# Kernel optimization log

Hardware: AMD Instinct MI355X
Metric: run time of the kernel (lower is better)

## Reference

```python
import jax, jax.numpy as jnp
import numpy as np

B, V = 256, 2048
PD, MD, H = 1024, 512, 512

def setup_inputs() -> dict:
    key = jax.random.key(0)
    k1, k2, k3, k4, k5 = jax.random.split(key, 5)
    patient_emb = jax.random.normal(k1, (B, PD), dtype=jnp.float32)
    atc4_emb = jax.random.normal(k2, (V, MD), dtype=jnp.float32)
    # Linear(PD+MD -> H): weight (H, PD+MD), bias (H,)
    W1 = jax.random.normal(k3, (H, PD + MD), dtype=jnp.float32) * 0.02
    b1 = jnp.zeros((H,), dtype=jnp.float32)
    # Linear(H -> 1): weight (1, H) -> store as (H,), bias scalar
    w2 = jax.random.normal(k4, (H,), dtype=jnp.float32) * 0.05
    b2 = jnp.zeros((), dtype=jnp.float32)
    return {"patient_emb": patient_emb, "atc4_emb": atc4_emb,
            "W1": W1, "b1": b1, "w2": w2, "b2": b2}

def reference(patient_emb, atc4_emb, W1, b1, w2, b2):
    # Algebraically equivalent to cat([patient, mol]) @ W1.T:
    # split W1 into patient and mol blocks, matmul each, broadcast-add.
    W1p = W1[:, :PD]   # (H, PD)
    W1m = W1[:, PD:]   # (H, MD)
    hp = jnp.einsum('bp,hp->bh', patient_emb, W1p)   # (B, H)
    hm = jnp.einsum('vm,hm->vh', atc4_emb, W1m)      # (V, H)
    h = jnp.tanh(hp[:, None, :] + hm[None, :, :] + b1)  # (B, V, H)
    scores = jnp.einsum('bvh,h->bv', h, w2) + b2     # (B, V)
    return scores
```

## Files before the change

### kernel.cpp

```cpp
#include <hip/hip_runtime.h>
#include <hip/hip_bf16.h>
#include <math.h>

typedef __attribute__((ext_vector_type(8))) short short8;
typedef __attribute__((ext_vector_type(4))) float float4v;
typedef __attribute__((ext_vector_type(2))) float float2v;

__device__ __forceinline__ float2v lo2(float4v v) {
    return __builtin_shufflevector(v, v, 0, 1);
}
__device__ __forceinline__ float2v hi2(float4v v) {
    return __builtin_shufflevector(v, v, 2, 3);
}

__device__ __forceinline__ int2 cvt2bf16x4(float4v v) {
    union { __hip_bfloat162 h2; int i; } u0, u1;
    u0.h2 = __float22bfloat162_rn(make_float2(v.x, v.y));
    u1.h2 = __float22bfloat162_rn(make_float2(v.z, v.w));
    return make_int2(u0.i, u1.i);
}

__global__ __launch_bounds__(256, 2) void gemm_exp(
    const float* __restrict__ patient, const float* __restrict__ atc4,
    const float* __restrict__ W1, const float* __restrict__ b1,
    float* __restrict__ EA, float* __restrict__ EM)
{
    const float* A; const float* W; const float* bias; float* T;
    int lda, K, M;
    int bx = blockIdx.x;
    if (bx < 4) {
        A = patient; lda = 1024; K = 1024; M = 256; bias = b1; T = EA; W = W1;
    } else {
        bx -= 4;
        A = atc4;    lda = 512;  K = 512;  M = 2048; bias = nullptr; T = EM; W = W1 + 1024;
    }
    const int ldw = 1536;

    __shared__ short As[64][72];
    __shared__ short Bs[64][72];
    const int t = threadIdx.x;
    const int m0 = bx * 64;
    const int n0 = blockIdx.y * 64;
    const int wave = t >> 6;
    const int lane = t & 63;
    const int wm = (wave & 1) * 32;
    const int wn = (wave >> 1) * 32;
    const int lrow = lane & 15;
    const int quad = lane >> 4;

    float4v acc[2][2];
    #pragma unroll
    for (int i = 0; i < 2; i++)
        #pragma unroll
        for (int j = 0; j < 2; j++)
            acc[i][j] = (float4v){0.f, 0.f, 0.f, 0.f};

    const int sr = t >> 2;
    const int sc = (t & 3) * 16;

    float4v av[4], wv[4];
    {
        const float* ap = A + (size_t)(m0 + sr) * lda + sc;
        const float* wp = W + (size_t)(n0 + sr) * ldw + sc;
        #pragma unroll
        for (int ii = 0; ii < 4; ii++) {
            av[ii] = *(const float4v*)(ap + ii * 4);
            wv[ii] = *(const float4v*)(wp + ii * 4);
        }
    }

    for (int k0 = 0; k0 < K; k0 += 64) {
        #pragma unroll
        for (int ii = 0; ii < 4; ii++) {
            *(int2*)&As[sr][sc + ii * 4] = cvt2bf16x4(av[ii]);
            *(int2*)&Bs[sr][sc + ii * 4] = cvt2bf16x4(wv[ii]);
        }
        __syncthreads();
        if (k0 + 64 < K) {
            const float* ap = A + (size_t)(m0 + sr) * lda + (k0 + 64 + sc);
            const float* wp = W + (size_t)(n0 + sr) * ldw + (k0 + 64 + sc);
            #pragma unroll
            for (int ii = 0; ii < 4; ii++) {
                av[ii] = *(const float4v*)(ap + ii * 4);
                wv[ii] = *(const float4v*)(wp + ii * 4);
            }
        }
        #pragma unroll
        for (int kk = 0; kk < 64; kk += 32) {
            short8 af[2], bfr[2];
            #pragma unroll
            for (int i = 0; i < 2; i++)
                af[i] = *(const short8*)&As[wm + i * 16 + lrow][kk + quad * 8];
            #pragma unroll
            for (int j = 0; j < 2; j++)
                bfr[j] = *(const short8*)&Bs[wn + j * 16 + lrow][kk + quad * 8];
            #pragma unroll
            for (int i = 0; i < 2; i++)
                #pragma unroll
                for (int j = 0; j < 2; j++)
                    acc[i][j] = __builtin_amdgcn_mfma_f32_16x16x32_bf16(
                        af[i], bfr[j], acc[i][j], 0, 0, 0);
        }
        __syncthreads();
    }

    #pragma unroll
    for (int i = 0; i < 2; i++) {
        #pragma unroll
        for (int j = 0; j < 2; j++) {
            const int n  = n0 + wn + j * 16 + lrow;
            const int mb = m0 + wm + i * 16 + quad * 4;
            const float bn = bias ? bias[n] : 0.0f;
            float4v ev;
            #pragma unroll
            for (int r = 0; r < 4; r++)
                ev[r] = __expf(2.0f * (acc[i][j][r] + bn));
            *(float4v*)&T[(size_t)n * M + mb] = ev;
        }
    }
}

__device__ __forceinline__ void rat4(
    float2v em0, float2v em1, float2v em2, float2v em3,
    float2v a0, float2v a1, float2v a2, float2v a3,
    float2v c0, float2v c1, float2v c2, float2v c3,
    float2v& acc)
{
    const float2v one2 = {1.f, 1.f};
    float2v d0 = __builtin_elementwise_fma(em0, a0, one2);
    float2v d1 = __builtin_elementwise_fma(em1, a1, one2);
    float2v d2 = __builtin_elementwise_fma(em2, a2, one2);
    float2v d3 = __builtin_elementwise_fma(em3, a3, one2);
    float2v e01 = d0 * d1;
    float2v e23 = d2 * d3;
    float2v n01 = __builtin_elementwise_fma(d1, c0, d0 * c1);
    float2v n23 = __builtin_elementwise_fma(d3, c2, d2 * c3);
    float2v num = __builtin_elementwise_fma(n01, e23, n23 * e01);
    float2v den = e01 * e23;
    float2v r = { __builtin_amdgcn_rcpf(den.x), __builtin_amdgcn_rcpf(den.y) };
    acc = __builtin_elementwise_fma(num, r, acc);
}

__global__ __launch_bounds__(256, 4) void pair_kernel(
    const float* __restrict__ EA, const float* __restrict__ EM,
    const float* __restrict__ w2, float* __restrict__ partial)
{
    __shared__ float sEA[32][68];
    __shared__ float sEM[32][132];
    __shared__ float4v sC4[8];
    const int t  = threadIdx.x;
    const int v0 = blockIdx.x * 128;
    const int b0 = blockIdx.y * 64;
    const int h0 = blockIdx.z * 32;
    const int tx = t & 15;
    const int ty = t >> 4;

    if (t < 8) {
        float4v wvq = *(const float4v*)(w2 + h0 + 4 * t);
        sC4[t] = -2.0f * wvq;
    }

    float2v accAL[4], accAH[4], accBL[4], accBH[4];
    #pragma unroll
    for (int i = 0; i < 4; i++) {
        accAL[i] = (float2v){0.f, 0.f};  accAH[i] = (float2v){0.f, 0.f};
        accBL[i] = (float2v){0.f, 0.f};  accBH[i] = (float2v){0.f, 0.f};
    }

    const int rS = t >> 3;
    const int cA = (t & 7) * 8;
    const int cM = (t & 7) * 16;

    {
        const float* pa = EA + (size_t)(h0 + rS) * 256 + b0 + cA;
        float4v pA0 = *(const float4v*)pa;
        float4v pA1 = *(const float4v*)(pa + 4);
        const float* pm = EM + (size_t)(h0 + rS) * 2048 + v0 + cM;
        float4v pM0 = *(const float4v*)pm;
        float4v pM1 = *(const float4v*)(pm + 4);
        float4v pM2 = *(const float4v*)(pm + 8);
        float4v pM3 = *(const float4v*)(pm + 12);
        *(float4v*)&sEA[rS][cA] = pA0;      *(float4v*)&sEA[rS][cA + 4] = pA1;
        *(float4v*)&sEM[rS][cM] = pM0;      *(float4v*)&sEM[rS][cM + 4] = pM1;
        *(float4v*)&sEM[rS][cM + 8] = pM2;  *(float4v*)&sEM[rS][cM + 12] = pM3;
    }
    __syncthreads();

    #pragma unroll 2
    for (int q = 0; q < 8; q++) {
        const int hq = 4 * q;
        const float4v ea0 = *(const float4v*)&sEA[hq    ][ty * 4];
        const float4v ea1 = *(const float4v*)&sEA[hq + 1][ty * 4];
        const float4v ea2 = *(const float4v*)&sEA[hq + 2][ty * 4];
        const float4v ea3 = *(const float4v*)&sEA[hq + 3][ty * 4];
        const float4v c = sC4[q];
        const float2v c0 = { c.x, c.x };
        const float2v c1 = { c.y, c.y };
        const float2v c2 = { c.z, c.z };
        const float2v c3 = { c.w, c.w };
        {
            const float4v em0 = *(const float4v*)&sEM[hq    ][tx * 4];
            const float4v em1 = *(const float4v*)&sEM[hq + 1][tx * 4];
            const float4v em2 = *(const float4v*)&sEM[hq + 2][tx * 4];
            const float4v em3 = *(const float4v*)&sEM[hq + 3][tx * 4];
            const float2v em0L = lo2(em0), em0H = hi2(em0);
            const float2v em1L = lo2(em1), em1H = hi2(em1);
            const float2v em2L = lo2(em2), em2H = hi2(em2);
            const float2v em3L = lo2(em3), em3H = hi2(em3);
            #pragma unroll
            for (int i = 0; i < 4; i++) {
                const float2v a0 = { ea0[i], ea0[i] };
                const float2v a1 = { ea1[i], ea1[i] };
                const float2v a2 = { ea2[i], ea2[i] };
                const float2v a3 = { ea3[i], ea3[i] };
                rat4(em0L, em1L, em2L, em3L, a0, a1, a2, a3,
                     c0, c1, c2, c3, accAL[i]);
                rat4(em0H, em1H, em2H, em3H, a0, a1, a2, a3,
                     c0, c1, c2, c3, accAH[i]);
            }
        }
        {
            const float4v em0 = *(const float4v*)&sEM[hq    ][64 + tx * 4];
            const float4v em1 = *(const float4v*)&sEM[hq + 1][64 + tx * 4];
            const float4v em2 = *(const float4v*)&sEM[hq + 2][64 + tx * 4];
            const float4v em3 = *(const float4v*)&sEM[hq + 3][64 + tx * 4];
            const float2v em0L = lo2(em0), em0H = hi2(em0);
            const float2v em1L = lo2(em1), em1H = hi2(em1);
            const float2v em2L = lo2(em2), em2H = hi2(em2);
            const float2v em3L = lo2(em3), em3H = hi2(em3);
            #pragma unroll
            for (int i = 0; i < 4; i++) {
                const float2v a0 = { ea0[i], ea0[i] };
                const float2v a1 = { ea1[i], ea1[i] };
                const float2v a2 = { ea2[i], ea2[i] };
                const float2v a3 = { ea3[i], ea3[i] };
                rat4(em0L, em1L, em2L, em3L, a0, a1, a2, a3,
                     c0, c1, c2, c3, accBL[i]);
                rat4(em0H, em1H, em2H, em3H, a0, a1, a2, a3,
                     c0, c1, c2, c3, accBH[i]);
            }
        }
    }

    float4v w2q = sC4[0];
    #pragma unroll
    for (int k = 1; k < 8; k++) w2q += sC4[k];
    const float w2s = -0.5f * (w2q.x + w2q.y + w2q.z + w2q.w);

    const size_t pb = (size_t)blockIdx.z * (256 * 2048);
    #pragma unroll
    for (int i = 0; i < 4; i++) {
        const size_t row = pb + (size_t)(b0 + ty * 4 + i) * 2048 + v0 + tx * 4;
        float4v oA = { accAL[i].x + w2s, accAL[i].y + w2s,
                       accAH[i].x + w2s, accAH[i].y + w2s };
        float4v oB = { accBL[i].x + w2s, accBL[i].y + w2s,
                       accBH[i].x + w2s, accBH[i].y + w2s };
        *(float4v*)&partial[row] = oA;
        *(float4v*)&partial[row + 64] = oB;
    }
}

__global__ __launch_bounds__(256) void reduce_kernel(
    const float* __restrict__ partial, const float* __restrict__ b2,
    float* __restrict__ out)
{
    const int i = (blockIdx.x * 256 + threadIdx.x) * 4;
    const float bb = b2[0];
    float4v s = *(const float4v*)&partial[i];
    #pragma unroll
    for (int z = 1; z < 16; z++)
        s += *(const float4v*)&partial[(size_t)z * 524288 + i];
    float4v o = s + bb;
    *(float4v*)&out[i] = o;
}

extern "C" void kernel_launch(void* const* d_in, const int* in_sizes, int n_in,
                              void* d_out, int out_size, void* d_ws, size_t ws_size,
                              hipStream_t stream)
{
    const float* patient = (const float*)d_in[0];
    const float* atc4    = (const float*)d_in[1];
    const float* W1      = (const float*)d_in[2];
    const float* b1      = (const float*)d_in[3];
    const float* w2      = (const float*)d_in[4];
    const float* b2      = (const float*)d_in[5];
    float* out = (float*)d_out;
    float* ws  = (float*)d_ws;

    float* EA      = ws;
    float* EM      = ws + 131072;
    float* partial = ws + 1179648;

    gemm_exp<<<dim3(36, 8, 1), 256, 0, stream>>>(patient, atc4, W1, b1, EA, EM);
    pair_kernel<<<dim3(16, 4, 16), 256, 0, stream>>>(EA, EM, w2, partial);
    reduce_kernel<<<512, 256, 0, stream>>>(partial, b2, out);
}
```

Baseline: 114.4 us.

## Double H-slice per pair block and software-pipeline EM shared-memory loads

Each pair_kernel block now covers 64 hidden units instead of 32, which halves the grid's z dimension and the number of partial-sum planes the reduce kernel must read and write. The inner loop prefetches the next quad's EM values from shared memory while the current quad computes, to hide LDS latency. In exchange, shared memory per block doubles to about 51 KB and register pressure rises, which may lower occupancy, and fewer blocks (512) may leave some CUs underused.

```diff
diff --git a/kernel.cpp b/kernel.cpp
--- a/kernel.cpp
+++ b/kernel.cpp
@@ -141,21 +141,42 @@
     acc = __builtin_elementwise_fma(num, r, acc);
 }
 
+__device__ __forceinline__ void quad_step(
+    float4v m0, float4v m1, float4v m2, float4v m3,
+    float4v ea0, float4v ea1, float4v ea2, float4v ea3,
+    float2v c0, float2v c1, float2v c2, float2v c3,
+    float2v (&accL)[4], float2v (&accH)[4])
+{
+    const float2v m0L = lo2(m0), m0H = hi2(m0);
+    const float2v m1L = lo2(m1), m1H = hi2(m1);
+    const float2v m2L = lo2(m2), m2H = hi2(m2);
+    const float2v m3L = lo2(m3), m3H = hi2(m3);
+    #pragma unroll
+    for (int i = 0; i < 4; i++) {
+        const float2v a0 = { ea0[i], ea0[i] };
+        const float2v a1 = { ea1[i], ea1[i] };
+        const float2v a2 = { ea2[i], ea2[i] };
+        const float2v a3 = { ea3[i], ea3[i] };
+        rat4(m0L, m1L, m2L, m3L, a0, a1, a2, a3, c0, c1, c2, c3, accL[i]);
+        rat4(m0H, m1H, m2H, m3H, a0, a1, a2, a3, c0, c1, c2, c3, accH[i]);
+    }
+}
+
 __global__ __launch_bounds__(256, 4) void pair_kernel(
     const float* __restrict__ EA, const float* __restrict__ EM,
     const float* __restrict__ w2, float* __restrict__ partial)
 {
-    __shared__ float sEA[32][68];
-    __shared__ float sEM[32][132];
-    __shared__ float4v sC4[8];
+    __shared__ float sEA[64][68];
+    __shared__ float sEM[64][132];
+    __shared__ float4v sC4[16];
     const int t  = threadIdx.x;
     const int v0 = blockIdx.x * 128;
     const int b0 = blockIdx.y * 64;
-    const int h0 = blockIdx.z * 32;
+    const int h0 = blockIdx.z * 64;
     const int tx = t & 15;
     const int ty = t >> 4;
 
-    if (t < 8) {
+    if (t < 16) {
         float4v wvq = *(const float4v*)(w2 + h0 + 4 * t);
         sC4[t] = -2.0f * wvq;
     }
@@ -167,28 +188,39 @@
         accBL[i] = (float2v){0.f, 0.f};  accBH[i] = (float2v){0.f, 0.f};
     }
 
-    const int rS = t >> 3;
-    const int cA = (t & 7) * 8;
-    const int cM = (t & 7) * 16;
-
     {
-        const float* pa = EA + (size_t)(h0 + rS) * 256 + b0 + cA;
-        float4v pA0 = *(const float4v*)pa;
-        float4v pA1 = *(const float4v*)(pa + 4);
-        const float* pm = EM + (size_t)(h0 + rS) * 2048 + v0 + cM;
-        float4v pM0 = *(const float4v*)pm;
-        float4v pM1 = *(const float4v*)(pm + 4);
-        float4v pM2 = *(const float4v*)(pm + 8);
-        float4v pM3 = *(const float4v*)(pm + 12);
-        *(float4v*)&sEA[rS][cA] = pA0;      *(float4v*)&sEA[rS][cA + 4] = pA1;
-        *(float4v*)&sEM[rS][cM] = pM0;      *(float4v*)&sEM[rS][cM + 4] = pM1;
-        *(float4v*)&sEM[rS][cM + 8] = pM2;  *(float4v*)&sEM[rS][cM + 12] = pM3;
+        const int rS = t >> 2;
+        const int cq = t & 3;
+        const float* pa = EA + (size_t)(h0 + rS) * 256 + b0 + cq * 16;
+        #pragma unroll
+        for (int i = 0; i < 4; i++) {
+            float4v v = *(const float4v*)(pa + 4 * i);
+            *(float4v*)&sEA[rS][cq * 16 + 4 * i] = v;
+        }
+        const float* pm = EM + (size_t)(h0 + rS) * 2048 + v0 + cq * 32;
+        #pragma unroll
+        for (int i = 0; i < 8; i++) {
+            float4v v = *(const float4v*)(pm + 4 * i);
+            *(float4v*)&sEM[rS][cq * 32 + 4 * i] = v;
+        }
     }
     __syncthreads();
 
-    #pragma unroll 2
-    for (int q = 0; q < 8; q++) {
+    const int cxA = tx * 4;
+    const int cxB = 64 + tx * 4;
+
+    float4v mA0 = *(const float4v*)&sEM[0][cxA];
+    float4v mA1 = *(const float4v*)&sEM[1][cxA];
+    float4v mA2 = *(const float4v*)&sEM[2][cxA];
+    float4v mA3 = *(const float4v*)&sEM[3][cxA];
+
+    #pragma unroll 4
+    for (int q = 0; q < 16; q++) {
         const int hq = 4 * q;
+        float4v mB0 = *(const float4v*)&sEM[hq    ][cxB];
+        float4v mB1 = *(const float4v*)&sEM[hq + 1][cxB];
+        float4v mB2 = *(const float4v*)&sEM[hq + 2][cxB];
+        float4v mB3 = *(const float4v*)&sEM[hq + 3][cxB];
         const float4v ea0 = *(const float4v*)&sEA[hq    ][ty * 4];
         const float4v ea1 = *(const float4v*)&sEA[hq + 1][ty * 4];
         const float4v ea2 = *(const float4v*)&sEA[hq + 2][ty * 4];
@@ -198,53 +230,25 @@
         const float2v c1 = { c.y, c.y };
         const float2v c2 = { c.z, c.z };
         const float2v c3 = { c.w, c.w };
-        {
-            const float4v em0 = *(const float4v*)&sEM[hq    ][tx * 4];
-            const float4v em1 = *(const float4v*)&sEM[hq + 1][tx * 4];
-            const float4v em2 = *(const float4v*)&sEM[hq + 2][tx * 4];
-            const float4v em3 = *(const float4v*)&sEM[hq + 3][tx * 4];
-            const float2v em0L = lo2(em0), em0H = hi2(em0);
-            const float2v em1L = lo2(em1), em1H = hi2(em1);
-            const float2v em2L = lo2(em2), em2H = hi2(em2);
-            const float2v em3L = lo2(em3), em3H = hi2(em3);
-            #pragma unroll
-            for (int i = 0; i < 4; i++) {
-                const float2v a0 = { ea0[i], ea0[i] };
-                const float2v a1 = { ea1[i], ea1[i] };
-                const float2v a2 = { ea2[i], ea2[i] };
-                const float2v a3 = { ea3[i], ea3[i] };
-                rat4(em0L, em1L, em2L, em3L, a0, a1, a2, a3,
-                     c0, c1, c2, c3, accAL[i]);
-                rat4(em0H, em1H, em2H, em3H, a0, a1, a2, a3,
-                     c0, c1, c2, c3, accAH[i]);
-            }
-        }
-        {
-            const float4v em0 = *(const float4v*)&sEM[hq    ][64 + tx * 4];
-            const float4v em1 = *(const float4v*)&sEM[hq + 1][64 + tx * 4];
-            const float4v em2 = *(const float4v*)&sEM[hq + 2][64 + tx * 4];
-            const float4v em3 = *(const float4v*)&sEM[hq + 3][64 + tx * 4];
-            const float2v em0L = lo2(em0), em0H = hi2(em0);
-            const float2v em1L = lo2(em1), em1H = hi2(em1);
-            const float2v em2L = lo2(em2), em2H = hi2(em2);
-            const float2v em3L = lo2(em3), em3H = hi2(em3);
-            #pragma unroll
-            for (int i = 0; i < 4; i++) {
-                const float2v a0 = { ea0[i], ea0[i] };
-                const float2v a1 = { ea1[i], ea1[i] };
-                const float2v a2 = { ea2[i], ea2[i] };
-                const float2v a3 = { ea3[i], ea3[i] };
-                rat4(em0L, em1L, em2L, em3L, a0, a1, a2, a3,
-                     c0, c1, c2, c3, accBL[i]);
-                rat4(em0H, em1H, em2H, em3H, a0, a1, a2, a3,
-                     c0, c1, c2, c3, accBH[i]);
-            }
-        }
+
+        quad_step(mA0, mA1, mA2, mA3, ea0, ea1, ea2, ea3,
+                  c0, c1, c2, c3, accAL, accAH);
+
+        const int hn = (hq + 4) & 63;
+        float4v nA0 = *(const float4v*)&sEM[hn    ][cxA];
+        float4v nA1 = *(const float4v*)&sEM[hn + 1][cxA];
+        float4v nA2 = *(const float4v*)&sEM[hn + 2][cxA];
+        float4v nA3 = *(const float4v*)&sEM[hn + 3][cxA];
+
+        quad_step(mB0, mB1, mB2, mB3, ea0, ea1, ea2, ea3,
+                  c0, c1, c2, c3, accBL, accBH);
+
+        mA0 = nA0; mA1 = nA1; mA2 = nA2; mA3 = nA3;
     }
 
     float4v w2q = sC4[0];
     #pragma unroll
-    for (int k = 1; k < 8; k++) w2q += sC4[k];
+    for (int k = 1; k < 16; k++) w2q += sC4[k];
     const float w2s = -0.5f * (w2q.x + w2q.y + w2q.z + w2q.w);
 
     const size_t pb = (size_t)blockIdx.z * (256 * 2048);
@@ -268,7 +272,7 @@
     const float bb = b2[0];
     float4v s = *(const float4v*)&partial[i];
     #pragma unroll
-    for (int z = 1; z < 16; z++)
+    for (int z = 1; z < 8; z++)
         s += *(const float4v*)&partial[(size_t)z * 524288 + i];
     float4v o = s + bb;
     *(float4v*)&out[i] = o;
@@ -292,6 +296,6 @@
     float* partial = ws + 1179648;
 
     gemm_exp<<<dim3(36, 8, 1), 256, 0, stream>>>(patient, atc4, W1, b1, EA, EM);
-    pair_kernel<<<dim3(16, 4, 16), 256, 0, stream>>>(EA, EM, w2, partial);
+    pair_kernel<<<dim3(16, 4, 8), 256, 0, stream>>>(EA, EM, w2, partial);
     reduce_kernel<<<512, 256, 0, stream>>>(partial, b2, out);
 }
```

New measurement: 113.0 us. Within noise of the previous version (-1.2%).
